# Kernel tuning notes

Hardware: AMD Instinct MI355X
Metric: run time of the kernel (lower is better)

The kernel has to match this reference:

```python
import jax, jax.numpy as jnp
import numpy as np

N = 100000   # nodes
E = 1600000  # edges
IN = 128     # input_dim
H = 64       # hidden_dim
C = 10       # num_classes
L = 4        # num_layers
G = 200      # graphs in batch
BN_EPS = 1e-5


def setup_inputs() -> dict:
    key = jax.random.key(0)
    ks = jax.random.split(key, 12)
    s = 0.05
    h = jax.random.normal(ks[0], (N, IN), jnp.float32)
    snorm_n = jax.random.uniform(ks[1], (N, 1), jnp.float32)
    src = jax.random.randint(ks[2], (E,), 0, N, jnp.int32)
    dst = jax.random.randint(ks[3], (E,), 0, N, jnp.int32)
    graph_ids = jnp.sort(jax.random.randint(ks[4], (N,), 0, G, jnp.int32))
    W_embed = jax.random.normal(ks[5], (IN, H), jnp.float32) * s
    b_embed = jnp.zeros((H,), jnp.float32)
    eps = jnp.zeros((L,), jnp.float32)               # learnable eps, init 0
    W1 = jax.random.normal(ks[6], (L, H, H), jnp.float32) * s
    b1 = jnp.zeros((L, H), jnp.float32)
    g1 = jnp.ones((L, H), jnp.float32)               # MLP-internal BN gamma
    be1 = jnp.zeros((L, H), jnp.float32)             # MLP-internal BN beta
    W2 = jax.random.normal(ks[7], (L, H, H), jnp.float32) * s
    b2 = jnp.zeros((L, H), jnp.float32)
    g2 = jnp.ones((L, H), jnp.float32)               # bn_node_h gamma
    be2 = jnp.zeros((L, H), jnp.float32)             # bn_node_h beta
    Wlin = jax.random.normal(ks[8], (L + 1, H, C), jnp.float32) * s
    blin = jnp.zeros((L + 1, C), jnp.float32)
    return dict(h=h, snorm_n=snorm_n, src=src, dst=dst, graph_ids=graph_ids,
                W_embed=W_embed, b_embed=b_embed, eps=eps,
                W1=W1, b1=b1, g1=g1, be1=be1, W2=W2, b2=b2, g2=g2, be2=be2,
                Wlin=Wlin, blin=blin)


def _batchnorm(x, gamma, beta):
    # training-mode BatchNorm1d over the node axis
    m = jnp.mean(x, axis=0)
    v = jnp.mean(jnp.square(x - m), axis=0)
    return gamma * (x - m) * jax.lax.rsqrt(v + BN_EPS) + beta


def reference(h, snorm_n, src, dst, graph_ids, W_embed, b_embed, eps,
              W1, b1, g1, be1, W2, b2, g2, be2, Wlin, blin):
    # node embedding
    h = h @ W_embed + b_embed                                   # [N, H]
    hidden_rep = [h]
    for i in range(L):
        h_in = h
        # copy_u + sum reduce: neigh[v] = sum_{(u->v)} h[u]
        neigh = jax.ops.segment_sum(h[src], dst, num_segments=N)  # [N, H]
        h = (1.0 + eps[i]) * h + neigh
        # apply_func: 2-layer MLP with internal BN+ReLU (standard GIN MLP)
        h = jax.nn.relu(_batchnorm(h @ W1[i] + b1[i], g1[i], be1[i]))
        h = h @ W2[i] + b2[i]
        h = h * snorm_n                                          # graph_norm
        h = _batchnorm(h, g2[i], be2[i])                         # bn_node_h
        h = jax.nn.relu(h)
        h = h_in + h                                             # residual
        # dropout p=0.0 -> identity
        hidden_rep.append(h)
    score = jnp.zeros((G, C), h.dtype)
    for i, hr in enumerate(hidden_rep):
        pooled = jax.ops.segment_sum(hr, graph_ids, num_segments=G)  # SumPooling
        score = score + pooled @ Wlin[i] + blin[i]
    return score
```

## Files before the change

### kernel.cpp

```cpp
#include <hip/hip_runtime.h>
#include <hip/hip_bf16.h>
#include <math.h>

#define NN 100000
#define NE 1600000
#define KIN 128
#define HD 64
#define NC 10
#define NL 4
#define NG 200
#define NBKT 196

typedef short s16x8 __attribute__((ext_vector_type(8)));
typedef float f32x4 __attribute__((ext_vector_type(4)));
using f4 = float4;

static __device__ __forceinline__ ushort f2bf(float x) {
  __hip_bfloat16 b = __float2bfloat16(x);
  return *reinterpret_cast<ushort*>(&b);
}
static __device__ __forceinline__ float bf2f(ushort u) {
  return __uint_as_float(((unsigned)u) << 16);
}
static __device__ __forceinline__ s16x8 zero8() {
  s16x8 v;
#pragma unroll
  for (int i = 0; i < 8; ++i) v[i] = 0;
  return v;
}

__global__ __launch_bounds__(256) void bucket_hist(const int* __restrict__ dst,
                                                   int* __restrict__ gbucket) {
  __shared__ int lh[NBKT];
  int tid = threadIdx.x;
  for (int i = tid; i < NBKT; i += 256) lh[i] = 0;
  __syncthreads();
  int base = blockIdx.x * 4096;
#pragma unroll 4
  for (int it = 0; it < 16; ++it) {
    int e = base + it * 256 + tid;
    if (e < NE) atomicAdd(&lh[dst[e] >> 9], 1);
  }
  __syncthreads();
  for (int i = tid; i < NBKT; i += 256)
    if (lh[i]) atomicAdd(&gbucket[i], lh[i]);
}

__global__ __launch_bounds__(256) void bucket_scan(const int* __restrict__ gbucket,
                                                   int* __restrict__ bbase,
                                                   int* __restrict__ bcur) {
  __shared__ int s[256];
  int tid = threadIdx.x;
  int v = (tid < NBKT) ? gbucket[tid] : 0;
  s[tid] = v;
  __syncthreads();
  for (int off = 1; off < 256; off <<= 1) {
    int t = (tid >= off) ? s[tid - off] : 0;
    __syncthreads();
    s[tid] += t;
    __syncthreads();
  }
  int excl = s[tid] - v;
  if (tid <= NBKT) bbase[tid] = excl;
  if (tid < NBKT) bcur[tid] = excl;
}

__global__ __launch_bounds__(256) void bucket_scatter(const int* __restrict__ src,
                                                      const int* __restrict__ dst,
                                                      int* __restrict__ bcur,
                                                      int2* __restrict__ pairs) {
  __shared__ int lh[NBKT];
  __shared__ int lbase[NBKT];
  int tid = threadIdx.x;
  for (int i = tid; i < NBKT; i += 256) lh[i] = 0;
  __syncthreads();
  int base = blockIdx.x * 4096;
  int dloc[16], sloc[16];
#pragma unroll
  for (int it = 0; it < 16; ++it) {
    int e = base + it * 256 + tid;
    bool ok = e < NE;
    dloc[it] = ok ? dst[e] : -1;
    sloc[it] = ok ? src[e] : 0;
    if (ok) atomicAdd(&lh[dloc[it] >> 9], 1);
  }
  __syncthreads();
  for (int i = tid; i < NBKT; i += 256) {
    int c = lh[i];
    lbase[i] = c ? atomicAdd(&bcur[i], c) : 0;
    lh[i] = 0;
  }
  __syncthreads();
#pragma unroll
  for (int it = 0; it < 16; ++it) {
    int d = dloc[it];
    if (d >= 0) {
      int b = d >> 9;
      int p = lbase[b] + atomicAdd(&lh[b], 1);
      pairs[p] = make_int2(d, sloc[it]);
    }
  }
}

__global__ __launch_bounds__(256) void csr_build(const int2* __restrict__ pairs,
                                                 const int* __restrict__ bbase,
                                                 int* __restrict__ row_ptr,
                                                 int* __restrict__ csr_src) {
  __shared__ int deg[512];
  __shared__ int psum[256];
  __shared__ int cur[512];
  int b = blockIdx.x;
  int tid = threadIdx.x;
  int beg = bbase[b], end = bbase[b + 1];
  int node0 = b << 9;
  deg[tid] = 0;
  deg[tid + 256] = 0;
  __syncthreads();
  for (int i = beg + tid; i < end; i += 256)
    atomicAdd(&deg[pairs[i].x - node0], 1);
  __syncthreads();
  int a0 = deg[2 * tid], a1 = deg[2 * tid + 1];
  psum[tid] = a0 + a1;
  __syncthreads();
  for (int off = 1; off < 256; off <<= 1) {
    int t = (tid >= off) ? psum[tid - off] : 0;
    __syncthreads();
    psum[tid] += t;
    __syncthreads();
  }
  int pe = psum[tid] - (a0 + a1);
  int e0 = pe, e1 = pe + a0;
  cur[2 * tid] = e0;
  cur[2 * tid + 1] = e1;
  int n0 = node0 + 2 * tid, n1 = node0 + 2 * tid + 1;
  if (n0 < NN) row_ptr[n0] = beg + e0;
  if (n1 < NN) row_ptr[n1] = beg + e1;
  __syncthreads();
  for (int i = beg + tid; i < end; i += 256) {
    int2 pr = pairs[i];
    int p = atomicAdd(&cur[pr.x - node0], 1);
    csr_src[beg + p] = pr.y;
  }
  if (b == 0 && tid == 0) row_ptr[NN] = NE;
}

__global__ __launch_bounds__(256) void pack_weights(
    const float* __restrict__ Wemb, const float* __restrict__ W1,
    const float* __restrict__ W2, ushort* __restrict__ Wpk) {
  int t = blockIdx.x;
  const float* src = (t < 2)   ? Wemb + t * 4096
                     : (t < 6) ? W1 + (t - 2) * 4096
                               : W2 + (t - 6) * 4096;
  for (int idx = threadIdx.x; idx < 4096; idx += 256) {
    int k = idx >> 6, n = idx & 63;
    int dsti = ((k >> 5) * 4 + (n >> 4)) * 512 +
               (((k >> 3) & 3) * 16 + (n & 15)) * 8 + (k & 7);
    Wpk[t * 4096 + dsti] = f2bf(src[idx]);
  }
}

__global__ __launch_bounds__(256) void pool_kernel(const ushort* __restrict__ hbf,
                                                   const int* __restrict__ gid,
                                                   float* __restrict__ pooledL) {
  int tid = threadIdx.x;
  int c = tid & 63;
  int rg = tid >> 6;
  int r0 = blockIdx.x * 128;
  int rend = r0 + 128 < NN ? r0 + 128 : NN;
  int rstart = r0 + rg;
  int cur = gid[rstart < NN ? rstart : NN - 1];
  float acc = 0.f;
  for (int r = rstart; r < rend; r += 4) {
    int g = gid[r];
    if (g != cur) {
      atomicAdd(&pooledL[cur * HD + c], acc);
      acc = 0.f;
      cur = g;
    }
    acc += bf2f(hbf[(size_t)r * HD + c]);
  }
  atomicAdd(&pooledL[cur * HD + c], acc);
}

template <int MODE, int MR, int BLK>
__global__ __launch_bounds__(BLK, (MODE == 1) ? 6 : 4) void gemm_kernel(
    const void* Xin, const ushort* __restrict__ wt,
    const float* __restrict__ bias, const float* __restrict__ bn_in,
    const float* __restrict__ g1p, const float* __restrict__ be1p,
    const float* __restrict__ snorm, const int* __restrict__ rp,
    const int* __restrict__ csrc, const float* __restrict__ eps_p,
    ushort* __restrict__ outbf, float* __restrict__ bn_out) {
  constexpr int NWAVE = BLK / 64;
  constexpr int WR = MR / NWAVE;
  constexpr int MI = WR / 16;
  __shared__ ushort lds_a[MR * 64];
  __shared__ ushort lds_b[4096];
  __shared__ float lds_red[2][NWAVE][64];
  __shared__ float lds_bn[2][64];

  const int tid = threadIdx.x;
  const int row0 = blockIdx.x * MR;
  const int w = tid >> 6;
  const int l = tid & 63;
  const int lr = l >> 4, lc = l & 15;

  if (MODE == 2) {
    if (tid < 64) {
      float s = bn_in[tid], q = bn_in[64 + tid];
      float m = s * (1.0f / NN);
      float r = rsqrtf(q * (1.0f / NN) - m * m + 1e-5f);
      float scl = g1p[tid] * r;
      lds_bn[0][tid] = scl;
      lds_bn[1][tid] = be1p[tid] - m * scl;
    }
    __syncthreads();
  }

  f32x4 acc[MI][4];
#pragma unroll
  for (int mi = 0; mi < MI; ++mi)
#pragma unroll
    for (int nf = 0; nf < 4; ++nf)
#pragma unroll
      for (int r = 0; r < 4; ++r) acc[mi][nf][r] = 0.f;

  const int KT = (MODE == 0) ? 2 : 1;
  for (int kt = 0; kt < KT; ++kt) {
    if (kt) __syncthreads();
#pragma unroll
    for (int i = 0; i < 512 / BLK; ++i) {
      int ch = i * BLK + tid;
      *reinterpret_cast<s16x8*>(&lds_b[ch * 8]) =
          *reinterpret_cast<const s16x8*>(&wt[kt * 4096 + ch * 8]);
    }
    if (MODE == 1) {
      const ushort* hbf = reinterpret_cast<const ushort*>(Xin);
      float epsv = 1.0f + eps_p[0];
      int lane = tid & 7;
#pragma unroll
      for (int g = 0; g < MR * 8 / BLK; ++g) {
        int row = g * (BLK / 8) + (tid >> 3);
        int grow = row0 + row;
        s16x8 val = zero8();
        if (grow < NN) {
          int beg = rp[grow], end = rp[grow + 1];
          f4 sv = *reinterpret_cast<const f4*>(&hbf[(size_t)grow * HD + lane * 8]);
          const ushort* su = reinterpret_cast<const ushort*>(&sv);
          float a8[8];
#pragma unroll
          for (int j = 0; j < 8; ++j) a8[j] = epsv * bf2f(su[j]);
          int e = beg;
          if (e + 1 < end) {
            f4 c0 = *reinterpret_cast<const f4*>(&hbf[(size_t)csrc[e] * HD + lane * 8]);
            f4 c1 = *reinterpret_cast<const f4*>(&hbf[(size_t)csrc[e + 1] * HD + lane * 8]);
            e += 2;
            while (e + 1 < end) {
              f4 n0 = *reinterpret_cast<const f4*>(&hbf[(size_t)csrc[e] * HD + lane * 8]);
              f4 n1 = *reinterpret_cast<const f4*>(&hbf[(size_t)csrc[e + 1] * HD + lane * 8]);
              e += 2;
              const ushort* u0 = reinterpret_cast<const ushort*>(&c0);
              const ushort* u1 = reinterpret_cast<const ushort*>(&c1);
#pragma unroll
              for (int j = 0; j < 8; ++j) a8[j] += bf2f(u0[j]) + bf2f(u1[j]);
              c0 = n0;
              c1 = n1;
            }
            const ushort* u0 = reinterpret_cast<const ushort*>(&c0);
            const ushort* u1 = reinterpret_cast<const ushort*>(&c1);
#pragma unroll
            for (int j = 0; j < 8; ++j) a8[j] += bf2f(u0[j]) + bf2f(u1[j]);
          }
          if (e < end) {
            f4 v0 = *reinterpret_cast<const f4*>(&hbf[(size_t)csrc[e] * HD + lane * 8]);
            const ushort* u0 = reinterpret_cast<const ushort*>(&v0);
#pragma unroll
            for (int j = 0; j < 8; ++j) a8[j] += bf2f(u0[j]);
          }
#pragma unroll
          for (int j = 0; j < 8; ++j) val[j] = (short)f2bf(a8[j]);
        }
        int slot = lane ^ (row & 7);
        *reinterpret_cast<s16x8*>(&lds_a[row * 64 + slot * 8]) = val;
      }
    } else {
#pragma unroll
      for (int i = 0; i < MR * 8 / BLK; ++i) {
        int f8i = i * BLK + tid;
        int row = f8i >> 3, c8 = f8i & 7;
        int grow = row0 + row;
        s16x8 val = zero8();
        if (grow < NN) {
          if (MODE == 0) {
            const float* p =
                reinterpret_cast<const float*>(Xin) + (size_t)grow * KIN + kt * 64 + c8 * 8;
            f4 x0 = *reinterpret_cast<const f4*>(p);
            f4 x1 = *reinterpret_cast<const f4*>(p + 4);
            float xv[8] = {x0.x, x0.y, x0.z, x0.w, x1.x, x1.y, x1.z, x1.w};
#pragma unroll
            for (int j = 0; j < 8; ++j) val[j] = (short)f2bf(xv[j]);
          } else {
            s16x8 raw = *reinterpret_cast<const s16x8*>(
                reinterpret_cast<const ushort*>(Xin) + (size_t)grow * HD + c8 * 8);
#pragma unroll
            for (int j = 0; j < 8; ++j) {
              int c = c8 * 8 + j;
              float v = bf2f((ushort)raw[j]) * lds_bn[0][c] + lds_bn[1][c];
              v = v > 0.f ? v : 0.f;
              val[j] = (short)f2bf(v);
            }
          }
        }
        int slot = c8 ^ (row & 7);
        *reinterpret_cast<s16x8*>(&lds_a[row * 64 + slot * 8]) = val;
      }
    }
    __syncthreads();

    s16x8 af[MI][2];
#pragma unroll
    for (int mi = 0; mi < MI; ++mi)
#pragma unroll
      for (int kh = 0; kh < 2; ++kh) {
        int row = w * WR + mi * 16 + lc;
        int slot = (kh * 4 + lr) ^ (row & 7);
        af[mi][kh] = *reinterpret_cast<const s16x8*>(&lds_a[row * 64 + slot * 8]);
      }
#pragma unroll
    for (int kh = 0; kh < 2; ++kh)
#pragma unroll
      for (int nf = 0; nf < 4; ++nf) {
        s16x8 bf = *reinterpret_cast<const s16x8*>(&lds_b[(kh * 4 + nf) * 512 + l * 8]);
#pragma unroll
        for (int mi = 0; mi < MI; ++mi)
          acc[mi][nf] = __builtin_amdgcn_mfma_f32_16x16x32_bf16(
              af[mi][kh], bf, acc[mi][nf], 0, 0, 0);
      }
  }

  float bias_l[4];
#pragma unroll
  for (int nf = 0; nf < 4; ++nf) bias_l[nf] = bias[nf * 16 + lc];

  float psum[4] = {0.f, 0.f, 0.f, 0.f}, psq[4] = {0.f, 0.f, 0.f, 0.f};
#pragma unroll
  for (int mi = 0; mi < MI; ++mi)
#pragma unroll
    for (int r = 0; r < 4; ++r) {
      int grow = row0 + w * WR + mi * 16 + lr * 4 + r;
      if (grow < NN) {
        float sn = (MODE == 2) ? snorm[grow] : 1.0f;
#pragma unroll
        for (int nf = 0; nf < 4; ++nf) {
          float v = acc[mi][nf][r] + bias_l[nf];
          if (MODE == 2) v *= sn;
          outbf[(size_t)grow * HD + nf * 16 + lc] = f2bf(v);
          if (MODE != 0) {
            psum[nf] += v;
            psq[nf] += v * v;
          }
        }
      }
    }
  if (MODE != 0) {
#pragma unroll
    for (int nf = 0; nf < 4; ++nf) {
      psum[nf] += __shfl_xor(psum[nf], 16);
      psq[nf] += __shfl_xor(psq[nf], 16);
      psum[nf] += __shfl_xor(psum[nf], 32);
      psq[nf] += __shfl_xor(psq[nf], 32);
    }
    if (l < 16) {
#pragma unroll
      for (int nf = 0; nf < 4; ++nf) {
        lds_red[0][w][nf * 16 + l] = psum[nf];
        lds_red[1][w][nf * 16 + l] = psq[nf];
      }
    }
    __syncthreads();
    if (tid < 64) {
      float s = 0.f, q = 0.f;
#pragma unroll
      for (int w2 = 0; w2 < NWAVE; ++w2) {
        s += lds_red[0][w2][tid];
        q += lds_red[1][w2][tid];
      }
      atomicAdd(&bn_out[tid], s);
      atomicAdd(&bn_out[64 + tid], q);
    }
  }
}

__global__ __launch_bounds__(256) void final_pool_kernel(
    const ushort* __restrict__ t2bf, ushort* __restrict__ hbf,
    const float* __restrict__ g2p, const float* __restrict__ be2p,
    const float* __restrict__ stats2, const int* __restrict__ gid,
    float* __restrict__ pooledL) {
  int tid = threadIdx.x;
  int c = tid & 63;
  int rg = tid >> 6;
  float s = stats2[c], q = stats2[64 + c];
  float m = s * (1.0f / NN);
  float rr = rsqrtf(q * (1.0f / NN) - m * m + 1e-5f);
  float scl = g2p[c] * rr;
  float shv = be2p[c] - m * scl;
  int r0 = blockIdx.x * 128;
  int rend = r0 + 128 < NN ? r0 + 128 : NN;
  int rstart = r0 + rg;
  int cur = gid[rstart < NN ? rstart : NN - 1];
  float pacc = 0.f;
  for (int r = rstart; r < rend; r += 4) {
    int g = gid[r];
    if (g != cur) {
      atomicAdd(&pooledL[cur * HD + c], pacc);
      pacc = 0.f;
      cur = g;
    }
    float v = bf2f(t2bf[(size_t)r * HD + c]) * scl + shv;
    v = v > 0.f ? v : 0.f;
    float nv = bf2f(hbf[(size_t)r * HD + c]) + v;
    hbf[(size_t)r * HD + c] = f2bf(nv);
    pacc += nv;
  }
  atomicAdd(&pooledL[cur * HD + c], pacc);
}

__global__ __launch_bounds__(256) void score_kernel(
    const float* __restrict__ pooled, const float* __restrict__ Wlin,
    const float* __restrict__ blin, float* __restrict__ out) {
  int o = blockIdx.x * 256 + threadIdx.x;
  if (o >= NG * NC) return;
  int g = o / NC, c = o % NC;
  float s = 0.f;
  for (int i = 0; i <= NL; ++i) {
    s += blin[i * NC + c];
    const float* pg = &pooled[i * NG * HD + g * HD];
    const float* wl = &Wlin[i * HD * NC + c];
    float acc = 0.f;
#pragma unroll 8
    for (int k = 0; k < HD; ++k) acc += pg[k] * wl[k * NC];
    s += acc;
  }
  out[o] = s;
}

extern "C" void kernel_launch(void* const* d_in, const int* in_sizes, int n_in,
                              void* d_out, int out_size, void* d_ws,
                              size_t ws_size, hipStream_t stream) {
  const float* X = (const float*)d_in[0];
  const float* snorm = (const float*)d_in[1];
  const int* src = (const int*)d_in[2];
  const int* dst = (const int*)d_in[3];
  const int* gid = (const int*)d_in[4];
  const float* W_embed = (const float*)d_in[5];
  const float* b_embed = (const float*)d_in[6];
  const float* eps = (const float*)d_in[7];
  const float* W1 = (const float*)d_in[8];
  const float* b1 = (const float*)d_in[9];
  const float* g1 = (const float*)d_in[10];
  const float* be1 = (const float*)d_in[11];
  const float* W2 = (const float*)d_in[12];
  const float* b2 = (const float*)d_in[13];
  const float* g2 = (const float*)d_in[14];
  const float* be2 = (const float*)d_in[15];
  const float* Wlin = (const float*)d_in[16];
  const float* blin = (const float*)d_in[17];

  float* ws = (float*)d_ws;
  float* scratch = ws;
  float* pooled = scratch + (size_t)NN * HD;
  float* stats = pooled + 5 * NG * HD;
  int* ib = (int*)(stats + NL * 256);
  int* row_ptr = ib;
  int* gbucket = ib + 100004;
  int* bbase = ib + 100200;
  int* bcur = ib + 100400;
  int* csr_src = ib + 100600;
  ushort* h_bf = (ushort*)(ib + 100600 + NE);
  ushort* t1bf = h_bf + (size_t)NN * HD;
  ushort* Wpk = t1bf + (size_t)NN * HD;
  int2* pairs = (int2*)scratch;

  const int GRID128 = (NN + 127) / 128;
  const int EBLK = (NE + 4095) / 4096;

  hipMemsetAsync(pooled, 0, (5 * NG * HD + NL * 256) * sizeof(float), stream);
  hipMemsetAsync(gbucket, 0, NBKT * sizeof(int), stream);

  pack_weights<<<10, 256, 0, stream>>>(W_embed, W1, W2, Wpk);

  bucket_hist<<<EBLK, 256, 0, stream>>>(dst, gbucket);
  bucket_scan<<<1, 256, 0, stream>>>(gbucket, bbase, bcur);
  bucket_scatter<<<EBLK, 256, 0, stream>>>(src, dst, bcur, pairs);
  csr_build<<<NBKT, 256, 0, stream>>>(pairs, bbase, row_ptr, csr_src);

  gemm_kernel<0, 128, 256><<<GRID128, 256, 0, stream>>>(
      X, Wpk, b_embed, nullptr, nullptr, nullptr, nullptr, nullptr, nullptr,
      nullptr, h_bf, nullptr);
  pool_kernel<<<GRID128, 256, 0, stream>>>(h_bf, gid, pooled);

  for (int l = 0; l < NL; ++l) {
    float* st1 = stats + l * 256;
    float* st2 = stats + l * 256 + 128;
    gemm_kernel<1, 128, 512><<<GRID128, 512, 0, stream>>>(
        h_bf, Wpk + (2 + l) * 4096, b1 + l * 64, nullptr, nullptr, nullptr,
        nullptr, row_ptr, csr_src, eps + l, t1bf, st1);
    gemm_kernel<2, 128, 256><<<GRID128, 256, 0, stream>>>(
        t1bf, Wpk + (6 + l) * 4096, b2 + l * 64, st1, g1 + l * 64,
        be1 + l * 64, snorm, nullptr, nullptr, nullptr, t1bf, st2);
    final_pool_kernel<<<GRID128, 256, 0, stream>>>(
        t1bf, h_bf, g2 + l * 64, be2 + l * 64, st2, gid,
        pooled + (l + 1) * NG * HD);
  }

  score_kernel<<<(NG * NC + 255) / 256, 256, 0, stream>>>(pooled, Wlin, blin,
                                                          (float*)d_out);
}
```

Measured before the change: 571.7 us.

## Fuse embedding GEMM with pooling and stage CSR indices in LDS

Replaces the separate embedding GEMM and pool kernels with one embed_kernel that writes bf16 activations and also stages them in LDS to do the first sum-pooling without re-reading global memory. The aggregation GEMM now preloads the block's contiguous CSR source indices into shared memory, falling back to global reads when a block has more than the staging capacity. It also merges the two memsets into one and lowers the aggregation kernel's occupancy hint from 6 to 4. The extra LDS and the lower occupancy hint may reduce the latency hiding available for the gather-heavy aggregation.

```diff
diff --git a/kernel.cpp b/kernel.cpp
--- a/kernel.cpp
+++ b/kernel.cpp
@@ -10,6 +10,7 @@
 #define NL 4
 #define NG 200
 #define NBKT 196
+#define MAXIDX 2560
 
 typedef short s16x8 __attribute__((ext_vector_type(8)));
 typedef float f32x4 __attribute__((ext_vector_type(4)));
@@ -159,31 +160,119 @@
   }
 }
 
-__global__ __launch_bounds__(256) void pool_kernel(const ushort* __restrict__ hbf,
-                                                   const int* __restrict__ gid,
-                                                   float* __restrict__ pooledL) {
-  int tid = threadIdx.x;
-  int c = tid & 63;
-  int rg = tid >> 6;
-  int r0 = blockIdx.x * 128;
-  int rend = r0 + 128 < NN ? r0 + 128 : NN;
-  int rstart = r0 + rg;
+__global__ __launch_bounds__(256, 4) void embed_kernel(
+    const float* __restrict__ X, const ushort* __restrict__ wt,
+    const float* __restrict__ bias, const int* __restrict__ gid,
+    ushort* __restrict__ hbf, float* __restrict__ pooled0) {
+  __shared__ ushort lds_a[128 * 64];
+  __shared__ ushort lds_b[4096];
+
+  const int tid = threadIdx.x;
+  const int row0 = blockIdx.x * 128;
+  const int w = tid >> 6;
+  const int l = tid & 63;
+  const int lr = l >> 4, lc = l & 15;
+
+  f32x4 acc[2][4];
+#pragma unroll
+  for (int mi = 0; mi < 2; ++mi)
+#pragma unroll
+    for (int nf = 0; nf < 4; ++nf)
+#pragma unroll
+      for (int r = 0; r < 4; ++r) acc[mi][nf][r] = 0.f;
+
+  for (int kt = 0; kt < 2; ++kt) {
+    if (kt) __syncthreads();
+#pragma unroll
+    for (int i = 0; i < 2; ++i) {
+      int ch = i * 256 + tid;
+      *reinterpret_cast<s16x8*>(&lds_b[ch * 8]) =
+          *reinterpret_cast<const s16x8*>(&wt[kt * 4096 + ch * 8]);
+    }
+#pragma unroll
+    for (int i = 0; i < 4; ++i) {
+      int f8i = i * 256 + tid;
+      int row = f8i >> 3, c8 = f8i & 7;
+      int grow = row0 + row;
+      s16x8 val = zero8();
+      if (grow < NN) {
+        const float* p = X + (size_t)grow * KIN + kt * 64 + c8 * 8;
+        f4 x0 = *reinterpret_cast<const f4*>(p);
+        f4 x1 = *reinterpret_cast<const f4*>(p + 4);
+        float xv[8] = {x0.x, x0.y, x0.z, x0.w, x1.x, x1.y, x1.z, x1.w};
+#pragma unroll
+        for (int j = 0; j < 8; ++j) val[j] = (short)f2bf(xv[j]);
+      }
+      int slot = c8 ^ (row & 7);
+      *reinterpret_cast<s16x8*>(&lds_a[row * 64 + slot * 8]) = val;
+    }
+    __syncthreads();
+
+    s16x8 af[2][2];
+#pragma unroll
+    for (int mi = 0; mi < 2; ++mi)
+#pragma unroll
+      for (int kh = 0; kh < 2; ++kh) {
+        int row = w * 32 + mi * 16 + lc;
+        int slot = (kh * 4 + lr) ^ (row & 7);
+        af[mi][kh] = *reinterpret_cast<const s16x8*>(&lds_a[row * 64 + slot * 8]);
+      }
+#pragma unroll
+    for (int kh = 0; kh < 2; ++kh)
+#pragma unroll
+      for (int nf = 0; nf < 4; ++nf) {
+        s16x8 bf = *reinterpret_cast<const s16x8*>(&lds_b[(kh * 4 + nf) * 512 + l * 8]);
+#pragma unroll
+        for (int mi = 0; mi < 2; ++mi)
+          acc[mi][nf] = __builtin_amdgcn_mfma_f32_16x16x32_bf16(
+              af[mi][kh], bf, acc[mi][nf], 0, 0, 0);
+      }
+  }
+
+  float bias_l[4];
+#pragma unroll
+  for (int nf = 0; nf < 4; ++nf) bias_l[nf] = bias[nf * 16 + lc];
+
+  __syncthreads();
+#pragma unroll
+  for (int mi = 0; mi < 2; ++mi)
+#pragma unroll
+    for (int r = 0; r < 4; ++r) {
+      int row = w * 32 + mi * 16 + lr * 4 + r;
+      int grow = row0 + row;
+      if (grow < NN) {
+#pragma unroll
+        for (int nf = 0; nf < 4; ++nf) {
+          float v = acc[mi][nf][r] + bias_l[nf];
+          ushort bv = f2bf(v);
+          int col = nf * 16 + lc;
+          hbf[(size_t)grow * HD + col] = bv;
+          lds_a[row * 64 + ((col >> 3) ^ (row & 7)) * 8 + (col & 7)] = bv;
+        }
+      }
+    }
+  __syncthreads();
+
+  int c = tid & 63, rg = tid >> 6;
+  int rend = row0 + 128 < NN ? row0 + 128 : NN;
+  int rstart = row0 + rg;
   int cur = gid[rstart < NN ? rstart : NN - 1];
-  float acc = 0.f;
+  float pacc = 0.f;
   for (int r = rstart; r < rend; r += 4) {
     int g = gid[r];
     if (g != cur) {
-      atomicAdd(&pooledL[cur * HD + c], acc);
-      acc = 0.f;
+      atomicAdd(&pooled0[cur * HD + c], pacc);
+      pacc = 0.f;
       cur = g;
     }
-    acc += bf2f(hbf[(size_t)r * HD + c]);
-  }
-  atomicAdd(&pooledL[cur * HD + c], acc);
+    int lrow = r - row0;
+    pacc += bf2f(lds_a[lrow * 64 + ((c >> 3) ^ (lrow & 7)) * 8 + (c & 7)]);
+  }
+  atomicAdd(&pooled0[cur * HD + c], pacc);
 }
 
 template <int MODE, int MR, int BLK>
-__global__ __launch_bounds__(BLK, (MODE == 1) ? 6 : 4) void gemm_kernel(
+__global__ __launch_bounds__(BLK, 4) void gemm_kernel(
     const void* Xin, const ushort* __restrict__ wt,
     const float* __restrict__ bias, const float* __restrict__ bn_in,
     const float* __restrict__ g1p, const float* __restrict__ be1p,
@@ -224,118 +313,115 @@
 #pragma unroll
       for (int r = 0; r < 4; ++r) acc[mi][nf][r] = 0.f;
 
-  const int KT = (MODE == 0) ? 2 : 1;
-  for (int kt = 0; kt < KT; ++kt) {
-    if (kt) __syncthreads();
-#pragma unroll
-    for (int i = 0; i < 512 / BLK; ++i) {
-      int ch = i * BLK + tid;
-      *reinterpret_cast<s16x8*>(&lds_b[ch * 8]) =
-          *reinterpret_cast<const s16x8*>(&wt[kt * 4096 + ch * 8]);
-    }
-    if (MODE == 1) {
-      const ushort* hbf = reinterpret_cast<const ushort*>(Xin);
-      float epsv = 1.0f + eps_p[0];
-      int lane = tid & 7;
-#pragma unroll
-      for (int g = 0; g < MR * 8 / BLK; ++g) {
-        int row = g * (BLK / 8) + (tid >> 3);
-        int grow = row0 + row;
-        s16x8 val = zero8();
-        if (grow < NN) {
-          int beg = rp[grow], end = rp[grow + 1];
-          f4 sv = *reinterpret_cast<const f4*>(&hbf[(size_t)grow * HD + lane * 8]);
-          const ushort* su = reinterpret_cast<const ushort*>(&sv);
-          float a8[8];
-#pragma unroll
-          for (int j = 0; j < 8; ++j) a8[j] = epsv * bf2f(su[j]);
-          int e = beg;
-          if (e + 1 < end) {
-            f4 c0 = *reinterpret_cast<const f4*>(&hbf[(size_t)csrc[e] * HD + lane * 8]);
-            f4 c1 = *reinterpret_cast<const f4*>(&hbf[(size_t)csrc[e + 1] * HD + lane * 8]);
+#pragma unroll
+  for (int i = 0; i < 512 / BLK; ++i) {
+    int ch = i * BLK + tid;
+    *reinterpret_cast<s16x8*>(&lds_b[ch * 8]) =
+        *reinterpret_cast<const s16x8*>(&wt[ch * 8]);
+  }
+
+  if (MODE == 1) {
+    __shared__ int lds_idx[MAXIDX];
+    const ushort* hbf = reinterpret_cast<const ushort*>(Xin);
+    float epsv = 1.0f + eps_p[0];
+    int lane = tid & 7;
+    int rhigh = row0 + MR < NN ? row0 + MR : NN;
+    int ebeg = rp[row0];
+    int ecnt = rp[rhigh] - ebeg;
+    int estg = ecnt < MAXIDX ? ecnt : MAXIDX;
+    for (int i = tid; i < estg; i += BLK) lds_idx[i] = csrc[ebeg + i];
+    __syncthreads();
+#pragma unroll
+    for (int g = 0; g < MR * 8 / BLK; ++g) {
+      int row = g * (BLK / 8) + (tid >> 3);
+      int grow = row0 + row;
+      s16x8 val = zero8();
+      if (grow < NN) {
+        int beg = rp[grow], end = rp[grow + 1];
+        bool uselds = (end - ebeg) <= MAXIDX;
+        f4 sv = *reinterpret_cast<const f4*>(&hbf[(size_t)grow * HD + lane * 8]);
+        const ushort* su = reinterpret_cast<const ushort*>(&sv);
+        float a8[8];
+#pragma unroll
+        for (int j = 0; j < 8; ++j) a8[j] = epsv * bf2f(su[j]);
+        int e = beg;
+#define EIDX(ee) (uselds ? lds_idx[(ee)-ebeg] : csrc[(ee)])
+        if (e + 1 < end) {
+          f4 c0 = *reinterpret_cast<const f4*>(&hbf[(size_t)EIDX(e) * HD + lane * 8]);
+          f4 c1 = *reinterpret_cast<const f4*>(&hbf[(size_t)EIDX(e + 1) * HD + lane * 8]);
+          e += 2;
+          while (e + 1 < end) {
+            f4 n0 = *reinterpret_cast<const f4*>(&hbf[(size_t)EIDX(e) * HD + lane * 8]);
+            f4 n1 = *reinterpret_cast<const f4*>(&hbf[(size_t)EIDX(e + 1) * HD + lane * 8]);
             e += 2;
-            while (e + 1 < end) {
-              f4 n0 = *reinterpret_cast<const f4*>(&hbf[(size_t)csrc[e] * HD + lane * 8]);
-              f4 n1 = *reinterpret_cast<const f4*>(&hbf[(size_t)csrc[e + 1] * HD + lane * 8]);
-              e += 2;
-              const ushort* u0 = reinterpret_cast<const ushort*>(&c0);
-              const ushort* u1 = reinterpret_cast<const ushort*>(&c1);
-#pragma unroll
-              for (int j = 0; j < 8; ++j) a8[j] += bf2f(u0[j]) + bf2f(u1[j]);
-              c0 = n0;
-              c1 = n1;
-            }
             const ushort* u0 = reinterpret_cast<const ushort*>(&c0);
             const ushort* u1 = reinterpret_cast<const ushort*>(&c1);
 #pragma unroll
             for (int j = 0; j < 8; ++j) a8[j] += bf2f(u0[j]) + bf2f(u1[j]);
+            c0 = n0;
+            c1 = n1;
           }
-          if (e < end) {
-            f4 v0 = *reinterpret_cast<const f4*>(&hbf[(size_t)csrc[e] * HD + lane * 8]);
-            const ushort* u0 = reinterpret_cast<const ushort*>(&v0);
-#pragma unroll
-            for (int j = 0; j < 8; ++j) a8[j] += bf2f(u0[j]);
-          }
-#pragma unroll
-          for (int j = 0; j < 8; ++j) val[j] = (short)f2bf(a8[j]);
+          const ushort* u0 = reinterpret_cast<const ushort*>(&c0);
+          const ushort* u1 = reinterpret_cast<const ushort*>(&c1);
+#pragma unroll
+          for (int j = 0; j < 8; ++j) a8[j] += bf2f(u0[j]) + bf2f(u1[j]);
         }
-        int slot = lane ^ (row & 7);
-        *reinterpret_cast<s16x8*>(&lds_a[row * 64 + slot * 8]) = val;
-      }
-    } else {
-#pragma unroll
-      for (int i = 0; i < MR * 8 / BLK; ++i) {
-        int f8i = i * BLK + tid;
-        int row = f8i >> 3, c8 = f8i & 7;
-        int grow = row0 + row;
-        s16x8 val = zero8();
-        if (grow < NN) {
-          if (MODE == 0) {
-            const float* p =
-                reinterpret_cast<const float*>(Xin) + (size_t)grow * KIN + kt * 64 + c8 * 8;
-            f4 x0 = *reinterpret_cast<const f4*>(p);
-            f4 x1 = *reinterpret_cast<const f4*>(p + 4);
-            float xv[8] = {x0.x, x0.y, x0.z, x0.w, x1.x, x1.y, x1.z, x1.w};
-#pragma unroll
-            for (int j = 0; j < 8; ++j) val[j] = (short)f2bf(xv[j]);
-          } else {
-            s16x8 raw = *reinterpret_cast<const s16x8*>(
-                reinterpret_cast<const ushort*>(Xin) + (size_t)grow * HD + c8 * 8);
-#pragma unroll
-            for (int j = 0; j < 8; ++j) {
-              int c = c8 * 8 + j;
-              float v = bf2f((ushort)raw[j]) * lds_bn[0][c] + lds_bn[1][c];
-              v = v > 0.f ? v : 0.f;
-              val[j] = (short)f2bf(v);
-            }
-          }
+        if (e < end) {
+          f4 v0 = *reinterpret_cast<const f4*>(&hbf[(size_t)EIDX(e) * HD + lane * 8]);
+          const ushort* u0 = reinterpret_cast<const ushort*>(&v0);
+#pragma unroll
+          for (int j = 0; j < 8; ++j) a8[j] += bf2f(u0[j]);
         }
-        int slot = c8 ^ (row & 7);
-        *reinterpret_cast<s16x8*>(&lds_a[row * 64 + slot * 8]) = val;
-      }
-    }
-    __syncthreads();
-
-    s16x8 af[MI][2];
-#pragma unroll
-    for (int mi = 0; mi < MI; ++mi)
-#pragma unroll
-      for (int kh = 0; kh < 2; ++kh) {
-        int row = w * WR + mi * 16 + lc;
-        int slot = (kh * 4 + lr) ^ (row & 7);
-        af[mi][kh] = *reinterpret_cast<const s16x8*>(&lds_a[row * 64 + slot * 8]);
-      }
-#pragma unroll
-    for (int kh = 0; kh < 2; ++kh)
-#pragma unroll
-      for (int nf = 0; nf < 4; ++nf) {
-        s16x8 bf = *reinterpret_cast<const s16x8*>(&lds_b[(kh * 4 + nf) * 512 + l * 8]);
-#pragma unroll
-        for (int mi = 0; mi < MI; ++mi)
-          acc[mi][nf] = __builtin_amdgcn_mfma_f32_16x16x32_bf16(
-              af[mi][kh], bf, acc[mi][nf], 0, 0, 0);
-      }
-  }
+#undef EIDX
+#pragma unroll
+        for (int j = 0; j < 8; ++j) val[j] = (short)f2bf(a8[j]);
+      }
+      int slot = lane ^ (row & 7);
+      *reinterpret_cast<s16x8*>(&lds_a[row * 64 + slot * 8]) = val;
+    }
+  } else {
+#pragma unroll
+    for (int i = 0; i < MR * 8 / BLK; ++i) {
+      int f8i = i * BLK + tid;
+      int row = f8i >> 3, c8 = f8i & 7;
+      int grow = row0 + row;
+      s16x8 val = zero8();
+      if (grow < NN) {
+        s16x8 raw = *reinterpret_cast<const s16x8*>(
+            reinterpret_cast<const ushort*>(Xin) + (size_t)grow * HD + c8 * 8);
+#pragma unroll
+        for (int j = 0; j < 8; ++j) {
+          int c = c8 * 8 + j;
+          float v = bf2f((ushort)raw[j]) * lds_bn[0][c] + lds_bn[1][c];
+          v = v > 0.f ? v : 0.f;
+          val[j] = (short)f2bf(v);
+        }
+      }
+      int slot = c8 ^ (row & 7);
+      *reinterpret_cast<s16x8*>(&lds_a[row * 64 + slot * 8]) = val;
+    }
+  }
+  __syncthreads();
+
+  s16x8 af[MI][2];
+#pragma unroll
+  for (int mi = 0; mi < MI; ++mi)
+#pragma unroll
+    for (int kh = 0; kh < 2; ++kh) {
+      int row = w * WR + mi * 16 + lc;
+      int slot = (kh * 4 + lr) ^ (row & 7);
+      af[mi][kh] = *reinterpret_cast<const s16x8*>(&lds_a[row * 64 + slot * 8]);
+    }
+#pragma unroll
+  for (int kh = 0; kh < 2; ++kh)
+#pragma unroll
+    for (int nf = 0; nf < 4; ++nf) {
+      s16x8 bf = *reinterpret_cast<const s16x8*>(&lds_b[(kh * 4 + nf) * 512 + l * 8]);
+#pragma unroll
+      for (int mi = 0; mi < MI; ++mi)
+        acc[mi][nf] = __builtin_amdgcn_mfma_f32_16x16x32_bf16(
+            af[mi][kh], bf, acc[mi][nf], 0, 0, 0);
+    }
 
   float bias_l[4];
 #pragma unroll
@@ -354,39 +440,35 @@
           float v = acc[mi][nf][r] + bias_l[nf];
           if (MODE == 2) v *= sn;
           outbf[(size_t)grow * HD + nf * 16 + lc] = f2bf(v);
-          if (MODE != 0) {
-            psum[nf] += v;
-            psq[nf] += v * v;
-          }
+          psum[nf] += v;
+          psq[nf] += v * v;
         }
       }
     }
-  if (MODE != 0) {
+#pragma unroll
+  for (int nf = 0; nf < 4; ++nf) {
+    psum[nf] += __shfl_xor(psum[nf], 16);
+    psq[nf] += __shfl_xor(psq[nf], 16);
+    psum[nf] += __shfl_xor(psum[nf], 32);
+    psq[nf] += __shfl_xor(psq[nf], 32);
+  }
+  if (l < 16) {
 #pragma unroll
     for (int nf = 0; nf < 4; ++nf) {
-      psum[nf] += __shfl_xor(psum[nf], 16);
-      psq[nf] += __shfl_xor(psq[nf], 16);
-      psum[nf] += __shfl_xor(psum[nf], 32);
-      psq[nf] += __shfl_xor(psq[nf], 32);
-    }
-    if (l < 16) {
-#pragma unroll
-      for (int nf = 0; nf < 4; ++nf) {
-        lds_red[0][w][nf * 16 + l] = psum[nf];
-        lds_red[1][w][nf * 16 + l] = psq[nf];
-      }
-    }
-    __syncthreads();
-    if (tid < 64) {
-      float s = 0.f, q = 0.f;
-#pragma unroll
-      for (int w2 = 0; w2 < NWAVE; ++w2) {
-        s += lds_red[0][w2][tid];
-        q += lds_red[1][w2][tid];
-      }
-      atomicAdd(&bn_out[tid], s);
-      atomicAdd(&bn_out[64 + tid], q);
-    }
+      lds_red[0][w][nf * 16 + l] = psum[nf];
+      lds_red[1][w][nf * 16 + l] = psq[nf];
+    }
+  }
+  __syncthreads();
+  if (tid < 64) {
+    float s = 0.f, q = 0.f;
+#pragma unroll
+    for (int w2 = 0; w2 < NWAVE; ++w2) {
+      s += lds_red[0][w2][tid];
+      q += lds_red[1][w2][tid];
+    }
+    atomicAdd(&bn_out[tid], s);
+    atomicAdd(&bn_out[64 + tid], q);
   }
 }
 
@@ -469,13 +551,13 @@
   float* scratch = ws;
   float* pooled = scratch + (size_t)NN * HD;
   float* stats = pooled + 5 * NG * HD;
-  int* ib = (int*)(stats + NL * 256);
+  int* gbucket = (int*)(stats + NL * 256);
+  int* ib = gbucket + 256;
   int* row_ptr = ib;
-  int* gbucket = ib + 100004;
-  int* bbase = ib + 100200;
-  int* bcur = ib + 100400;
-  int* csr_src = ib + 100600;
-  ushort* h_bf = (ushort*)(ib + 100600 + NE);
+  int* bbase = ib + 100004;
+  int* bcur = ib + 100204;
+  int* csr_src = ib + 100400;
+  ushort* h_bf = (ushort*)(ib + 100400 + NE);
   ushort* t1bf = h_bf + (size_t)NN * HD;
   ushort* Wpk = t1bf + (size_t)NN * HD;
   int2* pairs = (int2*)scratch;
@@ -483,8 +565,8 @@
   const int GRID128 = (NN + 127) / 128;
   const int EBLK = (NE + 4095) / 4096;
 
-  hipMemsetAsync(pooled, 0, (5 * NG * HD + NL * 256) * sizeof(float), stream);
-  hipMemsetAsync(gbucket, 0, NBKT * sizeof(int), stream);
+  hipMemsetAsync(pooled, 0, (5 * NG * HD + NL * 256 + 256) * sizeof(float),
+                 stream);
 
   pack_weights<<<10, 256, 0, stream>>>(W_embed, W1, W2, Wpk);
 
@@ -493,10 +575,8 @@
   bucket_scatter<<<EBLK, 256, 0, stream>>>(src, dst, bcur, pairs);
   csr_build<<<NBKT, 256, 0, stream>>>(pairs, bbase, row_ptr, csr_src);
 
-  gemm_kernel<0, 128, 256><<<GRID128, 256, 0, stream>>>(
-      X, Wpk, b_embed, nullptr, nullptr, nullptr, nullptr, nullptr, nullptr,
-      nullptr, h_bf, nullptr);
-  pool_kernel<<<GRID128, 256, 0, stream>>>(h_bf, gid, pooled);
+  embed_kernel<<<GRID128, 256, 0, stream>>>(X, Wpk, b_embed, gid, h_bf,
+                                            pooled);
 
   for (int l = 0; l < NL; ++l) {
     float* st1 = stats + l * 256;
```

After: 560.2 us. -2.0%, faster.
